# Optimization experiments

Hardware: AMD Instinct MI355X
Metric: run time of the kernel (lower is better)

Reference implementation:

```python
import jax, jax.numpy as jnp
import numpy as np

N, D, NUM_CLASSES = 8192, 64, 16
EPS = 1e-7


def setup_inputs() -> dict:
    key = jax.random.key(0)
    k1, k2 = jax.random.split(key)
    raw = jax.random.normal(k1, (N, D), dtype=jnp.float32)
    # project into the open Poincare ball: norm < 0.9
    nrm = jnp.linalg.norm(raw, axis=-1, keepdims=True)
    points = raw * (0.9 / (1.0 + nrm))
    labels = jax.random.randint(k2, (N,), 0, NUM_CLASSES, dtype=jnp.int64)
    return {"points": points, "labels": labels}


def _poincare_dist_matrix(x):
    # d(x,y) = arccosh(1 + 2||x-y||^2 / ((1-||x||^2)(1-||y||^2)))
    sq = jnp.sum(x * x, axis=-1)                      # [N]
    sqdist = jnp.maximum(sq[:, None] + sq[None, :] - 2.0 * (x @ x.T), 0.0)  # [N,N]
    denom = jnp.maximum((1.0 - sq)[:, None] * (1.0 - sq)[None, :], EPS)
    arg = jnp.maximum(1.0 + 2.0 * sqdist / denom, 1.0 + EPS)
    return jnp.arccosh(arg)


def reference(points, labels):
    d = _poincare_dist_matrix(points)                 # [N,N]
    logits = -d
    n = logits.shape[0]
    diag = jnp.eye(n, dtype=bool)
    neg_inf = jnp.finfo(logits.dtype).min
    # log A_i = logsumexp_{a != i} (-d_ia)
    logA = jax.nn.logsumexp(jnp.where(diag, neg_inf, logits), axis=1)  # [N]
    pos = (labels[:, None] == labels[None, :]) & (~diag)               # [N,N]
    P = jnp.sum(pos, axis=1).astype(logits.dtype)                      # [N]
    p_sum = jnp.sum(jnp.where(pos, logits - logA[:, None], 0.0), axis=1)
    return jnp.sum(-p_sum / P)
```

## Files before the change

kernel.cpp:

```cpp
#include <hip/hip_runtime.h>

#define NPTS 8192
#define DIM 64
#define EPSF 1e-7f
#define LN2F 0.69314718055994531f
#define NBLK 1056

typedef unsigned short u16;
typedef __attribute__((ext_vector_type(8))) short bf16x8;
typedef __attribute__((ext_vector_type(8))) unsigned short u16x8;
typedef __attribute__((ext_vector_type(4))) float f32x4;
typedef __attribute__((ext_vector_type(2))) float f32x2;

__global__ void prep_kernel(const float* __restrict__ x, const int* __restrict__ labels,
                            u16* __restrict__ hi,
                            float4* __restrict__ meta,
                            float* __restrict__ S, float* __restrict__ T,
                            float* __restrict__ out) {
    int g = blockIdx.x * blockDim.x + threadIdx.x;
    int row = g >> 3, sub = g & 7;
    const float* xp = x + row * DIM + sub * 8;
    float v[8];
    float s = 0.f;
#pragma unroll
    for (int k = 0; k < 8; k++) { v[k] = xp[k]; s = fmaf(v[k], v[k], s); }
    s += __shfl_xor(s, 1);
    s += __shfl_xor(s, 2);
    s += __shfl_xor(s, 4);
    u16x8 h;
#pragma unroll
    for (int k = 0; k < 8; k++) {
        unsigned int bits = __float_as_uint(v[k]);
        unsigned int r = bits + 0x7FFFu + ((bits >> 16) & 1u);
        h[k] = (u16)(r >> 16);
    }
    *(u16x8*)(hi + row * DIM + sub * 8) = h;
    if (sub == 0) {
        float r = 1.0f / (1.0f - s);
        meta[row] = make_float4(-0.5f * s, r, -4.0f * r, (float)labels[row]);
    } else if (sub == 1) {
        S[row] = 0.f;
    } else if (sub == 2) {
        T[row] = 0.f;
    }
    if (g == 3) out[0] = 0.f;
}

__device__ __forceinline__ int cumtiles(int b) { return 65 * b - b * b; }

__global__ void __launch_bounds__(256, 4) pair_mfma(
        const u16* __restrict__ hi,
        const float4* __restrict__ meta,
        float* __restrict__ Sarr, float* __restrict__ Tarr) {
    __shared__ f32x2 slab[4][4][128];

    int tid = threadIdx.x;
    int wave = tid >> 6, lane = tid & 63;
    int quad = lane >> 4, l15 = lane & 15;

    int bid2 = blockIdx.x;
    int bid = bid2 >> 1;
    int half = bid2 & 1;
    int by = (int)((65.0f - __builtin_amdgcn_sqrtf(4225.0f - 4.0f * (float)bid)) * 0.5f);
    while (cumtiles(by + 1) <= bid) by++;
    while (cumtiles(by) > bid) by--;
    int off = bid - cumtiles(by);
    int bx = 2 * by + off;
    bool full = (off >= 2);

    int i0 = bx * 128 + wave * 32;
    int j0 = by * 256;
    int jbase = j0 + half * 128;

    bf16x8 a_hi[2][2];
#pragma unroll
    for (int it = 0; it < 2; it++)
#pragma unroll
        for (int ks = 0; ks < 2; ks++) {
            int aoff = (i0 + it * 16 + l15) * DIM + ks * 32 + quad * 8;
            a_hi[it][ks] = *(const bf16x8*)(hi + aoff);
        }

    f32x4 hsqi4[2];
    f32x2 rcp2[4];
    float labi[8];
#pragma unroll
    for (int it = 0; it < 2; it++)
#pragma unroll
        for (int r = 0; r < 4; r++) {
            float4 m = meta[i0 + it * 16 + quad * 4 + r];
            hsqi4[it][r] = m.x;
            rcp2[it * 2 + (r >> 1)][r & 1] = m.y;
            labi[it * 4 + r] = m.w;
        }

    f32x2 Sx2[4], Tx2[4];
#pragma unroll
    for (int k = 0; k < 4; k++) { Sx2[k] = (f32x2){0.f, 0.f}; Tx2[k] = (f32x2){0.f, 0.f}; }

    bf16x8 bh[2][2];
    float4 mjb[2];
    {
        int boff = (jbase + l15) * DIM + quad * 8;
        bh[0][0] = *(const bf16x8*)(hi + boff);
        bh[0][1] = *(const bf16x8*)(hi + boff + 32);
        mjb[0] = meta[jbase + l15];
    }

#pragma unroll 2
    for (int t = 0; t < 8; t++) {
        int cur = t & 1, nxt = cur ^ 1;
        if (t < 7) {
            int jgn = jbase + (t + 1) * 16 + l15;
            int boff = jgn * DIM + quad * 8;
            bh[nxt][0] = *(const bf16x8*)(hi + boff);
            bh[nxt][1] = *(const bf16x8*)(hi + boff + 32);
            mjb[nxt] = meta[jgn];
        }
        float4 mj = mjb[cur];

        f32x2 sSum = (f32x2){0.f, 0.f}, tSum = (f32x2){0.f, 0.f};
#pragma unroll
        for (int it = 0; it < 2; it++) {
            f32x4 acc = hsqi4[it] + mj.x;
            acc = __builtin_amdgcn_mfma_f32_16x16x32_bf16(a_hi[it][0], bh[cur][0], acc, 0, 0, 0);
            acc = __builtin_amdgcn_mfma_f32_16x16x32_bf16(a_hi[it][1], bh[cur][1], acc, 0, 0, 0);

#pragma unroll
            for (int g = 0; g < 2; g++) {
                f32x2 D = (f32x2){acc[2 * g], acc[2 * g + 1]};
                f32x2 u = (D * rcp2[it * 2 + g]) * mj.z;
                u = __builtin_elementwise_max(u, (f32x2){EPSF, EPSF});
                f32x2 arg = u * u + (u + u);
                f32x2 srt = (f32x2){__builtin_amdgcn_sqrtf(arg.x), __builtin_amdgcn_sqrtf(arg.y)};
                f32x2 opu = u + 1.0f;
                f32x2 st = opu - srt;
                f32x2 w1 = opu + srt;
                f32x2 l2;
                l2.x = __builtin_amdgcn_logf(w1.x);
                l2.y = __builtin_amdgcn_logf(w1.y);
                f32x2 tv;
                tv.x = (mj.w == labi[it * 4 + 2 * g]) ? l2.x : 0.0f;
                tv.y = (mj.w == labi[it * 4 + 2 * g + 1]) ? l2.y : 0.0f;
                Sx2[it * 2 + g] += st;
                Tx2[it * 2 + g] += tv;
                sSum += st;
                tSum += tv;
            }
        }

        slab[wave][quad][t * 16 + l15] = (f32x2){sSum.x + sSum.y, tSum.x + tSum.y};
    }

    float Sx[8], Tx[8];
#pragma unroll
    for (int k = 0; k < 4; k++) {
        Sx[2 * k] = Sx2[k].x; Sx[2 * k + 1] = Sx2[k].y;
        Tx[2 * k] = Tx2[k].x; Tx[2 * k + 1] = Tx2[k].y;
    }
#pragma unroll
    for (int r = 0; r < 8; r++) {
#pragma unroll
        for (int m = 1; m < 16; m <<= 1) {
            Sx[r] += __shfl_xor(Sx[r], m);
            Tx[r] += __shfl_xor(Tx[r], m);
        }
    }
    if (l15 == 0) {
#pragma unroll
        for (int it = 0; it < 2; it++)
#pragma unroll
            for (int r = 0; r < 4; r++) {
                int row = i0 + it * 16 + quad * 4 + r;
                atomicAdd(&Sarr[row], Sx[it * 4 + r]);
                atomicAdd(&Tarr[row], Tx[it * 4 + r]);
            }
    }

    if (full) {
        __syncthreads();
        int c = tid & 127, h = tid >> 7;
        f32x2 a2 = (f32x2){0.f, 0.f};
#pragma unroll
        for (int w = 0; w < 2; w++)
#pragma unroll
            for (int q = 0; q < 4; q++)
                a2 += slab[h * 2 + w][q][c];
        atomicAdd(&Sarr[jbase + c], a2.x);
        atomicAdd(&Tarr[jbase + c], a2.y);
    }
}

__global__ void __launch_bounds__(256) finalize_kernel(
        const float* __restrict__ S, const float* __restrict__ T,
        const int* __restrict__ labels, float* __restrict__ out) {
    __shared__ int hist[16][16];
    __shared__ float cntf[16];
    __shared__ float red[256];
    int tid = threadIdx.x;
    hist[tid >> 4][tid & 15] = 0;
    __syncthreads();
    int rep = tid & 15;
    for (int i = tid; i < NPTS; i += 256)
        atomicAdd(&hist[rep][labels[i]], 1);
    __syncthreads();
    if (tid < 16) {
        int s = 0;
#pragma unroll
        for (int k = 0; k < 16; k++) s += hist[k][tid];
        cntf[tid] = (float)(s - 1);
    }
    __syncthreads();

    float s0 = __builtin_amdgcn_sqrtf(EPSF * (2.0f + EPSF));
    float st0 = 1.0f + EPSF - s0;
    float l20 = __builtin_amdgcn_logf(1.0f + EPSF + s0);
    int i = blockIdx.x * 256 + tid;
    float loss = __logf(S[i] - st0) + (T[i] - l20) * LN2F / cntf[labels[i]];
    red[tid] = loss;
    __syncthreads();
    for (int s = 128; s > 0; s >>= 1) {
        if (tid < s) red[tid] += red[tid + s];
        __syncthreads();
    }
    if (tid == 0) atomicAdd(out, red[0]);
}

extern "C" void kernel_launch(void* const* d_in, const int* in_sizes, int n_in,
                              void* d_out, int out_size, void* d_ws, size_t ws_size,
                              hipStream_t stream) {
    const float* x = (const float*)d_in[0];
    const int* labels = (const int*)d_in[1];

    u16* hi = (u16*)d_ws;
    float4* meta = (float4*)(hi + NPTS * DIM);
    float* S = (float*)(meta + NPTS);
    float* T = S + NPTS;

    prep_kernel<<<(NPTS * 8) / 256, 256, 0, stream>>>(x, labels, hi, meta, S, T, (float*)d_out);

    pair_mfma<<<2 * NBLK, 256, 0, stream>>>(hi, meta, S, T);

    finalize_kernel<<<NPTS / 256, 256, 0, stream>>>(S, T, labels, (float*)d_out);
}
```

Baseline: 105.2 us.

## Stage B tile and metadata in LDS via direct global-to-LDS loads

Each block now loads its 128-row B tile of bf16 points and the matching metadata into shared memory up front with global_load_lds, using an XOR swizzle so the per-iteration reads avoid bank conflicts. This replaces the per-wave register double-buffered global loads. The column-partial slab is also reorganised: quads combine into per-wave LDS arrays with shared-memory atomics, so the final reduction is shorter. The cost is an extra __syncthreads before compute, with no overlap between the tile load and the first MFMAs, plus LDS atomic traffic.

```diff
diff --git a/kernel.cpp b/kernel.cpp
--- a/kernel.cpp
+++ b/kernel.cpp
@@ -11,6 +11,11 @@
 typedef __attribute__((ext_vector_type(8))) unsigned short u16x8;
 typedef __attribute__((ext_vector_type(4))) float f32x4;
 typedef __attribute__((ext_vector_type(2))) float f32x2;
+
+#define GLOAD_LDS(gsrc, ldst)                                                  \
+    __builtin_amdgcn_global_load_lds(                                          \
+        (const __attribute__((address_space(1))) unsigned int*)(gsrc),         \
+        (__attribute__((address_space(3))) unsigned int*)(ldst), 16, 0, 0)
 
 __global__ void prep_kernel(const float* __restrict__ x, const int* __restrict__ labels,
                             u16* __restrict__ hi,
@@ -52,7 +57,9 @@
         const u16* __restrict__ hi,
         const float4* __restrict__ meta,
         float* __restrict__ Sarr, float* __restrict__ Tarr) {
-    __shared__ f32x2 slab[4][4][128];
+    __shared__ u16x8 Bl8[128 * 8];
+    __shared__ float4 Ml[128];
+    __shared__ float slabS[4][128], slabT[4][128];
 
     int tid = threadIdx.x;
     int wave = tid >> 6, lane = tid & 63;
@@ -69,8 +76,21 @@
     bool full = (off >= 2);
 
     int i0 = bx * 128 + wave * 32;
-    int j0 = by * 256;
-    int jbase = j0 + half * 128;
+    int jbase = by * 256 + half * 128;
+
+    {
+        int rin = lane >> 3, cch = lane & 7;
+#pragma unroll
+        for (int q = 0; q < 4; q++) {
+            int r = wave * 32 + q * 8 + rin;
+            const u16* src = hi + (size_t)(jbase + r) * DIM + ((cch ^ (r & 7)) << 3);
+            GLOAD_LDS(src, &Bl8[(wave * 32 + q * 8) * 8]);
+        }
+        if (wave < 2) {
+            const float4* msrc = meta + jbase + wave * 64 + lane;
+            GLOAD_LDS(msrc, &Ml[wave * 64]);
+        }
+    }
 
     bf16x8 a_hi[2][2];
 #pragma unroll
@@ -94,37 +114,32 @@
             labi[it * 4 + r] = m.w;
         }
 
+    ((float*)slabS)[tid] = 0.f; ((float*)slabS)[tid + 256] = 0.f;
+    ((float*)slabT)[tid] = 0.f; ((float*)slabT)[tid + 256] = 0.f;
+
+    __syncthreads();
+
     f32x2 Sx2[4], Tx2[4];
 #pragma unroll
     for (int k = 0; k < 4; k++) { Sx2[k] = (f32x2){0.f, 0.f}; Tx2[k] = (f32x2){0.f, 0.f}; }
 
-    bf16x8 bh[2][2];
-    float4 mjb[2];
-    {
-        int boff = (jbase + l15) * DIM + quad * 8;
-        bh[0][0] = *(const bf16x8*)(hi + boff);
-        bh[0][1] = *(const bf16x8*)(hi + boff + 32);
-        mjb[0] = meta[jbase + l15];
-    }
+    int swz0 = (quad ^ (l15 & 7)) << 4;
+    int swz1 = ((quad + 4) ^ (l15 & 7)) << 4;
+    const char* Bb = (const char*)Bl8;
 
 #pragma unroll 2
     for (int t = 0; t < 8; t++) {
-        int cur = t & 1, nxt = cur ^ 1;
-        if (t < 7) {
-            int jgn = jbase + (t + 1) * 16 + l15;
-            int boff = jgn * DIM + quad * 8;
-            bh[nxt][0] = *(const bf16x8*)(hi + boff);
-            bh[nxt][1] = *(const bf16x8*)(hi + boff + 32);
-            mjb[nxt] = meta[jgn];
-        }
-        float4 mj = mjb[cur];
+        int r = t * 16 + l15;
+        float4 mj = Ml[r];
+        bf16x8 b0 = *(const bf16x8*)(Bb + r * 128 + swz0);
+        bf16x8 b1 = *(const bf16x8*)(Bb + r * 128 + swz1);
 
         f32x2 sSum = (f32x2){0.f, 0.f}, tSum = (f32x2){0.f, 0.f};
 #pragma unroll
         for (int it = 0; it < 2; it++) {
             f32x4 acc = hsqi4[it] + mj.x;
-            acc = __builtin_amdgcn_mfma_f32_16x16x32_bf16(a_hi[it][0], bh[cur][0], acc, 0, 0, 0);
-            acc = __builtin_amdgcn_mfma_f32_16x16x32_bf16(a_hi[it][1], bh[cur][1], acc, 0, 0, 0);
+            acc = __builtin_amdgcn_mfma_f32_16x16x32_bf16(a_hi[it][0], b0, acc, 0, 0, 0);
+            acc = __builtin_amdgcn_mfma_f32_16x16x32_bf16(a_hi[it][1], b1, acc, 0, 0, 0);
 
 #pragma unroll
             for (int g = 0; g < 2; g++) {
@@ -149,7 +164,8 @@
             }
         }
 
-        slab[wave][quad][t * 16 + l15] = (f32x2){sSum.x + sSum.y, tSum.x + tSum.y};
+        atomicAdd(&slabS[wave][r], sSum.x + sSum.y);
+        atomicAdd(&slabT[wave][r], tSum.x + tSum.y);
     }
 
     float Sx[8], Tx[8];
@@ -179,15 +195,14 @@
 
     if (full) {
         __syncthreads();
-        int c = tid & 127, h = tid >> 7;
-        f32x2 a2 = (f32x2){0.f, 0.f};
-#pragma unroll
-        for (int w = 0; w < 2; w++)
-#pragma unroll
-            for (int q = 0; q < 4; q++)
-                a2 += slab[h * 2 + w][q][c];
-        atomicAdd(&Sarr[jbase + c], a2.x);
-        atomicAdd(&Tarr[jbase + c], a2.y);
+        if (tid < 128) {
+            float s = slabS[0][tid] + slabS[1][tid] + slabS[2][tid] + slabS[3][tid];
+            atomicAdd(&Sarr[jbase + tid], s);
+        } else {
+            int c = tid - 128;
+            float tt = slabT[0][c] + slabT[1][c] + slabT[2][c] + slabT[3][c];
+            atomicAdd(&Tarr[jbase + c], tt);
+        }
     }
 }
 
```

New measurement: 125.5 us. 19.2% more time.
